# Kernel tuning notes

Measured on AMD Instinct MI355X. Metric: run time of the kernel, lower is better.

The kernel has to match this reference:

```python
import jax, jax.numpy as jnp
import numpy as np

B, S, U, H = 4, 2048, 1024, 16
DH = U // H  # head dim = 64
EPS = 1e-8


def setup_inputs() -> dict:
    key = jax.random.key(0)
    ks = jax.random.split(key, 7)
    scale = 1.0 / np.sqrt(U)
    return {
        "queries": jax.random.normal(ks[0], (B, S, U), jnp.float32),
        "keys": jax.random.normal(ks[1], (B, S, U), jnp.float32),
        "values": jax.random.normal(ks[2], (B, S, U), jnp.float32),
        "Wq": jax.random.normal(ks[3], (U, U), jnp.float32) * scale,
        "bq": jnp.zeros((U,), jnp.float32),
        "Wk": jax.random.normal(ks[4], (U, U), jnp.float32) * scale,
        "bk": jnp.zeros((U,), jnp.float32),
        "Wv": jax.random.normal(ks[5], (U, U), jnp.float32) * scale,
        "bv": jnp.zeros((U,), jnp.float32),
        "Wr": jax.random.normal(ks[6], (U, U), jnp.float32) * scale,
        "br": jnp.zeros((U,), jnp.float32),
        "gamma": jnp.ones((U,), jnp.float32),
        "beta": jnp.zeros((U,), jnp.float32),
    }


def reference(queries, keys, values, Wq, bq, Wk, bk, Wv, bv, Wr, br, gamma, beta):
    relu = jax.nn.relu
    Q = relu(queries @ Wq + bq)           # [B,S,U]
    K = relu(keys @ Wk + bk)
    V = relu(values @ Wv + bv)
    V_res = relu(values @ Wr + br)        # residual branch

    # split heads: tf.split(axis=2) + concat(axis=0) == per-head attention
    Qh = Q.reshape(B, S, H, DH)
    Kh = K.reshape(B, S, H, DH)
    Vh = V.reshape(B, S, H, DH)

    scores = jnp.einsum("bshd,bthd->bhst", Qh, Kh) / jnp.sqrt(jnp.float32(DH))
    w = jax.nn.softmax(scores, axis=-1)   # dropout keep_prob=1 -> identity
    out = jnp.einsum("bhst,bthd->bshd", w, Vh).reshape(B, S, U)

    out = relu(out + V_res)

    # manual LayerNorm (eps inside sqrt)
    mean = jnp.mean(out, axis=-1, keepdims=True)
    var = jnp.mean(jnp.square(out - mean), axis=-1, keepdims=True)
    normalized = (out - mean) / jnp.sqrt(var + EPS)
    return gamma * normalized + beta
```

## Files before the change

kernel.cpp:

```cpp
#include <hip/hip_runtime.h>

constexpr int B = 4, S = 2048, U = 1024, H = 16, DH = 64;
constexpr int MTOT = B * S;
constexpr int NT = S / 64;

using bf16   = __bf16;
using f32x4  = __attribute__((ext_vector_type(4))) float;
using f32x16 = __attribute__((ext_vector_type(16))) float;
using bf16x8 = __attribute__((ext_vector_type(8))) bf16;
using bf16x4 = __attribute__((ext_vector_type(4))) bf16;
using u32x4  = __attribute__((ext_vector_type(4))) unsigned int;

__device__ __forceinline__ void gload16(const bf16* g, bf16* l) {
  __builtin_amdgcn_global_load_lds(
      (const __attribute__((address_space(1))) unsigned int*)g,
      (__attribute__((address_space(3))) unsigned int*)l, 16, 0, 0);
}

__device__ __forceinline__ float fexp2(float x) {
#if __has_builtin(__builtin_amdgcn_exp2f)
  return __builtin_amdgcn_exp2f(x);
#else
  return __expf(x * 0.6931471805599453f);
#endif
}

__device__ __forceinline__ f32x16 mfma32(bf16x8 a, bf16x8 b, f32x16 c) {
  return __builtin_amdgcn_mfma_f32_32x32x16_bf16(a, b, c, 0, 0, 0);
}

__device__ __forceinline__ unsigned packbf(float a, float b) {
  union { bf16 h; unsigned short s; } ua, ub;
  ua.h = (bf16)a; ub.h = (bf16)b;
  return ((unsigned)ub.s << 16) | (unsigned)ua.s;
}

__device__ __forceinline__ size_t kpack_off(int M_, int col) {
  const int b = M_ >> 11, s = M_ & 2047;
  const int h = col >> 6, d = col & 63;
  const int bh = b * 16 + h;
  const int t = s >> 6, r64 = s & 63;
  const int tt = r64 >> 5, l31 = r64 & 31;
  const int ks = d >> 4, hi = (d >> 3) & 1, j = d & 7;
  const int ln = l31 + (hi << 5);
  return ((size_t)(bh * 32 + t) << 12) + (tt << 11) + (ks << 9) + (ln << 3) + j;
}

__device__ __forceinline__ size_t vpack_off(int M_, int col) {
  const int b = M_ >> 11, s = M_ & 2047;
  const int h = col >> 6, d = col & 63;
  const int bh = b * 16 + h;
  const int j = s & 7, hi = (s >> 3) & 1, ks = (s >> 4) & 3, t = s >> 6;
  const int dt = d >> 5, l31 = d & 31;
  const int ln = l31 + (hi << 5);
  return ((size_t)(bh * 32 + t) << 12) + (dt << 11) + (ks << 9) + (ln << 3) + j;
}

__global__ __launch_bounds__(256) void prep_kernel(
    const float* __restrict__ xq, const float* __restrict__ xk, const float* __restrict__ xv,
    bf16* __restrict__ oq, bf16* __restrict__ ok, bf16* __restrict__ ov,
    const float* __restrict__ w0, const float* __restrict__ w1,
    const float* __restrict__ w2, const float* __restrict__ w3,
    bf16* __restrict__ t0, bf16* __restrict__ t1,
    bf16* __restrict__ t2, bf16* __restrict__ t3) {
  __shared__ float tile[32][33];
  const int bid = blockIdx.x;
  const int t = threadIdx.x;
  if (bid < 12288) {
    const int z = bid >> 12, idx = bid & 4095;
    const float* x = z == 0 ? xq : z == 1 ? xk : xv;
    bf16* o       = z == 0 ? oq : z == 1 ? ok : ov;
    const size_t i = ((size_t)idx * 256 + t) * 8;
    const float4 v0 = *reinterpret_cast<const float4*>(x + i);
    const float4 v1 = *reinterpret_cast<const float4*>(x + i + 4);
    bf16x8 r;
    r[0] = (bf16)v0.x; r[1] = (bf16)v0.y; r[2] = (bf16)v0.z; r[3] = (bf16)v0.w;
    r[4] = (bf16)v1.x; r[5] = (bf16)v1.y; r[6] = (bf16)v1.z; r[7] = (bf16)v1.w;
    *reinterpret_cast<bf16x8*>(o + i) = r;
  } else {
    const int wb = bid - 12288;
    const int z = wb >> 10, ti = wb & 1023;
    const float* W = z == 0 ? w0 : z == 1 ? w1 : z == 2 ? w2 : w3;
    bf16* Wt       = z == 0 ? t0 : z == 1 ? t1 : z == 2 ? t2 : t3;
    const int k0 = (ti & 31) * 32, n0 = (ti >> 5) * 32;
    const int tx = t & 31, ty = t >> 5;
    for (int i = ty; i < 32; i += 8) tile[i][tx] = W[(size_t)(k0 + i) * U + n0 + tx];
    __syncthreads();
    for (int i = ty; i < 32; i += 8) Wt[(size_t)(n0 + i) * U + k0 + tx] = (bf16)tile[tx][i];
  }
}

__global__ __launch_bounds__(512, 2) void gemm4_kernel(
    const bf16* __restrict__ Qc, const bf16* __restrict__ Kc, const bf16* __restrict__ Vc,
    const bf16* __restrict__ wqt, const bf16* __restrict__ wkt,
    const bf16* __restrict__ wvt, const bf16* __restrict__ wrt,
    const float* __restrict__ bq, const float* __restrict__ bk,
    const float* __restrict__ bv, const float* __restrict__ br,
    bf16* __restrict__ oq, bf16* __restrict__ okp,
    bf16* __restrict__ ovp, bf16* __restrict__ orr) {
  const int bid = blockIdx.x;
  const int wg = (bid & 7) * 64 + (bid >> 3);
  const int z = wg >> 7, rem = wg & 127;
  const int bm = (rem >> 2) * 256, bn = (rem & 3) * 256;

  const bf16* A     = z == 0 ? Qc : z == 1 ? Kc : Vc;
  const bf16* Wt    = z == 0 ? wqt : z == 1 ? wkt : z == 2 ? wvt : wrt;
  const float* bias = z == 0 ? bq : z == 1 ? bk : z == 2 ? bv : br;

  const int tid = threadIdx.x, lane = tid & 63, w = tid >> 6;
  const int wr = w >> 2, wcn = w & 3;
  const int lm = lane & 15, hi = lane >> 4;

  __shared__ __align__(16) bf16 smem[65536];

  f32x4 acc[8][4];
#pragma unroll
  for (int i = 0; i < 8; ++i)
#pragma unroll
    for (int j = 0; j < 4; ++j) acc[i][j] = f32x4{0.f, 0.f, 0.f, 0.f};

  const int srow = tid >> 3, sslot = tid & 7;
  const int scol = (sslot ^ (srow & 7)) * 8;
  const bf16* gA = A  + (size_t)(bm + srow) * U + scol;
  const bf16* gB = Wt + (size_t)(bn + srow) * U + scol;

  auto stageA = [&](int buf, int half, int k0) {
    bf16* l = smem + buf * 32768 + (half * 128 + srow) * 64 + sslot * 8;
    gload16(gA + (size_t)(half * 128) * U + k0, l);
    gload16(gA + (size_t)(half * 128 + 64) * U + k0, l + 64 * 64);
  };
  auto stageB = [&](int buf, int half, int k0) {
    bf16* l = smem + buf * 32768 + 16384 + (half * 128 + srow) * 64 + sslot * 8;
    gload16(gB + (size_t)(half * 128) * U + k0, l);
    gload16(gB + (size_t)(half * 128 + 64) * U + k0, l + 64 * 64);
  };

  auto loadA = [&](int buf, int mi, int ks) {
    const int row = wr * 128 + mi * 16 + lm;
    const int slot = (ks * 4 + hi) ^ (lm & 7);
    return *reinterpret_cast<const bf16x8*>(smem + buf * 32768 + row * 64 + slot * 8);
  };
  auto loadB = [&](int buf, int ni, int ks) {
    const int row = wcn * 64 + ni * 16 + lm;
    const int slot = (ks * 4 + hi) ^ (lm & 7);
    return *reinterpret_cast<const bf16x8*>(smem + buf * 32768 + 16384 + row * 64 + slot * 8);
  };

  stageA(0, 0, 0); stageA(0, 1, 0); stageB(0, 0, 0); stageB(0, 1, 0);
  asm volatile("s_waitcnt vmcnt(0)" ::: "memory");
  __builtin_amdgcn_s_barrier();
  __builtin_amdgcn_sched_barrier(0);

  for (int t = 0; t < 16; ++t) {
    const int buf = t & 1, nbf = buf ^ 1;
    const int k1 = (t + 1) * 64;
    const bool pre = (t + 1) < 16;

    bf16x8 bfr[4][2];

    if (pre) stageA(nbf, 0, k1);
#pragma unroll
    for (int ni = 0; ni < 4; ++ni) {
      bfr[ni][0] = loadB(buf, ni, 0);
      bfr[ni][1] = loadB(buf, ni, 1);
    }
    {
      bf16x8 a00 = loadA(buf, 0, 0), a01 = loadA(buf, 0, 1);
      bf16x8 a10 = loadA(buf, 1, 0), a11 = loadA(buf, 1, 1);
      __builtin_amdgcn_s_setprio(1);
#pragma unroll
      for (int ni = 0; ni < 4; ++ni) {
        acc[0][ni] = __builtin_amdgcn_mfma_f32_16x16x32_bf16(a00, bfr[ni][0], acc[0][ni], 0, 0, 0);
        acc[0][ni] = __builtin_amdgcn_mfma_f32_16x16x32_bf16(a01, bfr[ni][1], acc[0][ni], 0, 0, 0);
        acc[1][ni] = __builtin_amdgcn_mfma_f32_16x16x32_bf16(a10, bfr[ni][0], acc[1][ni], 0, 0, 0);
        acc[1][ni] = __builtin_amdgcn_mfma_f32_16x16x32_bf16(a11, bfr[ni][1], acc[1][ni], 0, 0, 0);
      }
      __builtin_amdgcn_s_setprio(0);
    }
    if (pre) stageA(nbf, 1, k1);
    {
      bf16x8 a00 = loadA(buf, 2, 0), a01 = loadA(buf, 2, 1);
      bf16x8 a10 = loadA(buf, 3, 0), a11 = loadA(buf, 3, 1);
      __builtin_amdgcn_s_setprio(1);
#pragma unroll
      for (int ni = 0; ni < 4; ++ni) {
        acc[2][ni] = __builtin_amdgcn_mfma_f32_16x16x32_bf16(a00, bfr[ni][0], acc[2][ni], 0, 0, 0);
        acc[2][ni] = __builtin_amdgcn_mfma_f32_16x16x32_bf16(a01, bfr[ni][1], acc[2][ni], 0, 0, 0);
        acc[3][ni] = __builtin_amdgcn_mfma_f32_16x16x32_bf16(a10, bfr[ni][0], acc[3][ni], 0, 0, 0);
        acc[3][ni] = __builtin_amdgcn_mfma_f32_16x16x32_bf16(a11, bfr[ni][1], acc[3][ni], 0, 0, 0);
      }
      __builtin_amdgcn_s_setprio(0);
    }
    if (pre) stageB(nbf, 0, k1);
    {
      bf16x8 a00 = loadA(buf, 4, 0), a01 = loadA(buf, 4, 1);
      bf16x8 a10 = loadA(buf, 5, 0), a11 = loadA(buf, 5, 1);
      __builtin_amdgcn_s_setprio(1);
#pragma unroll
      for (int ni = 0; ni < 4; ++ni) {
        acc[4][ni] = __builtin_amdgcn_mfma_f32_16x16x32_bf16(a00, bfr[ni][0], acc[4][ni], 0, 0, 0);
        acc[4][ni] = __builtin_amdgcn_mfma_f32_16x16x32_bf16(a01, bfr[ni][1], acc[4][ni], 0, 0, 0);
        acc[5][ni] = __builtin_amdgcn_mfma_f32_16x16x32_bf16(a10, bfr[ni][0], acc[5][ni], 0, 0, 0);
        acc[5][ni] = __builtin_amdgcn_mfma_f32_16x16x32_bf16(a11, bfr[ni][1], acc[5][ni], 0, 0, 0);
      }
      __builtin_amdgcn_s_setprio(0);
    }
    if (pre) stageB(nbf, 1, k1);
    {
      bf16x8 a00 = loadA(buf, 6, 0), a01 = loadA(buf, 6, 1);
      bf16x8 a10 = loadA(buf, 7, 0), a11 = loadA(buf, 7, 1);
      __builtin_amdgcn_s_setprio(1);
#pragma unroll
      for (int ni = 0; ni < 4; ++ni) {
        acc[6][ni] = __builtin_amdgcn_mfma_f32_16x16x32_bf16(a00, bfr[ni][0], acc[6][ni], 0, 0, 0);
        acc[6][ni] = __builtin_amdgcn_mfma_f32_16x16x32_bf16(a01, bfr[ni][1], acc[6][ni], 0, 0, 0);
        acc[7][ni] = __builtin_amdgcn_mfma_f32_16x16x32_bf16(a10, bfr[ni][0], acc[7][ni], 0, 0, 0);
        acc[7][ni] = __builtin_amdgcn_mfma_f32_16x16x32_bf16(a11, bfr[ni][1], acc[7][ni], 0, 0, 0);
      }
      __builtin_amdgcn_s_setprio(0);
    }

    if (pre) {
      asm volatile("s_waitcnt vmcnt(0)" ::: "memory");
      __builtin_amdgcn_s_barrier();
      __builtin_amdgcn_sched_barrier(0);
    }
  }

  const int mb = bm + wr * 128 + hi * 4;
  const int nb = bn + wcn * 64 + lm;
  if (z == 1) {
#pragma unroll
    for (int ni = 0; ni < 4; ++ni) {
      const float bv_ = bias[nb + ni * 16];
#pragma unroll
      for (int mi = 0; mi < 8; ++mi)
#pragma unroll
        for (int r = 0; r < 4; ++r) {
          const float vv = fmaxf(acc[mi][ni][r] + bv_, 0.f);
          okp[kpack_off(mb + mi * 16 + r, nb + ni * 16)] = (bf16)vv;
        }
    }
  } else if (z == 2) {
#pragma unroll
    for (int ni = 0; ni < 4; ++ni) {
      const float bv_ = bias[nb + ni * 16];
#pragma unroll
      for (int mi = 0; mi < 8; ++mi)
#pragma unroll
        for (int r = 0; r < 4; ++r) {
          const float vv = fmaxf(acc[mi][ni][r] + bv_, 0.f);
          ovp[vpack_off(mb + mi * 16 + r, nb + ni * 16)] = (bf16)vv;
        }
    }
  } else {
    bf16* out = z == 0 ? oq : orr;
#pragma unroll
    for (int ni = 0; ni < 4; ++ni) {
      const float bv_ = bias[nb + ni * 16];
#pragma unroll
      for (int mi = 0; mi < 8; ++mi)
#pragma unroll
        for (int r = 0; r < 4; ++r) {
          const float vv = fmaxf(acc[mi][ni][r] + bv_, 0.f);
          out[(size_t)(mb + mi * 16 + r) * U + nb + ni * 16] = (bf16)vv;
        }
    }
  }
}

__global__ __launch_bounds__(256, 2) void attn_kernel(
    const bf16* __restrict__ Q, const bf16* __restrict__ Kp,
    const bf16* __restrict__ Vp, bf16* __restrict__ att) {
  const int bid = blockIdx.x;
  const int swz = (bid & 7) * 128 + (bid >> 3);
  const int bh = swz >> 4, qx = swz & 15;
  const int b = bh >> 4, h = bh & 15;
  const int tid = threadIdx.x;
  const int w = tid >> 6, lane = tid & 63;
  const int l31 = lane & 31, hi8 = lane >> 5;
  const int q0 = qx * 128 + w * 32;

  __shared__ __align__(16) bf16 kv[2][8192];

  const float qscale = 0.18033688011111606f;

  const bf16* qbase = Q + ((size_t)b * S + q0 + l31) * U + h * DH + hi8 * 8;
  bf16x8 qf[4];
#pragma unroll
  for (int ks = 0; ks < 4; ++ks) {
    bf16x8 v = *reinterpret_cast<const bf16x8*>(qbase + ks * 16);
#pragma unroll
    for (int j = 0; j < 8; ++j) v[j] = (bf16)((float)v[j] * qscale);
    qf[ks] = v;
  }

  bf16x8 onesf;
#pragma unroll
  for (int j = 0; j < 8; ++j) onesf[j] = (bf16)1.f;

  f32x16 o0 = (f32x16)0.f, o1 = (f32x16)0.f, osum = (f32x16)0.f;

  const bf16* kpb = Kp + (size_t)bh * 32 * 4096;
  const bf16* vpb = Vp + (size_t)bh * 32 * 4096;

  auto stagekv = [&](int buf, int t) {
    const size_t toff = (size_t)t * 4096;
    gload16(kpb + toff + tid * 8,        &kv[buf][tid * 8]);
    gload16(kpb + toff + 2048 + tid * 8, &kv[buf][2048 + tid * 8]);
    gload16(vpb + toff + tid * 8,        &kv[buf][4096 + tid * 8]);
    gload16(vpb + toff + 2048 + tid * 8, &kv[buf][6144 + tid * 8]);
  };

  stagekv(0, 0);
  asm volatile("s_waitcnt vmcnt(0)" ::: "memory");
  __builtin_amdgcn_s_barrier();
  __builtin_amdgcn_sched_barrier(0);

  for (int t = 0; t < NT; ++t) {
    const int cur = t & 1;
    if (t + 1 < NT) stagekv(cur ^ 1, t + 1);

    bf16x8 kf[2][4];
#pragma unroll
    for (int tt = 0; tt < 2; ++tt)
#pragma unroll
      for (int ks = 0; ks < 4; ++ks)
        kf[tt][ks] = *reinterpret_cast<const bf16x8*>(&kv[cur][(tt * 4 + ks) * 512 + lane * 8]);

    f32x16 s0 = (f32x16)0.f, s1 = (f32x16)0.f;
    __builtin_amdgcn_s_setprio(1);
#pragma unroll
    for (int ks = 0; ks < 4; ++ks) {
      s0 = mfma32(kf[0][ks], qf[ks], s0);
      s1 = mfma32(kf[1][ks], qf[ks], s1);
    }
    __builtin_amdgcn_s_setprio(0);

    bf16x8 vf[2][4];
#pragma unroll
    for (int dt = 0; dt < 2; ++dt)
#pragma unroll
      for (int ks = 0; ks < 4; ++ks)
        vf[dt][ks] = *reinterpret_cast<const bf16x8*>(&kv[cur][4096 + (dt * 4 + ks) * 512 + lane * 8]);

    unsigned wpk[16];
#pragma unroll
    for (int i = 0; i < 8; ++i) {
      wpk[i]     = packbf(fexp2(s0[2 * i]), fexp2(s0[2 * i + 1]));
      wpk[8 + i] = packbf(fexp2(s1[2 * i]), fexp2(s1[2 * i + 1]));
    }

    u32x4 fw[4];
#pragma unroll
    for (int fi = 0; fi < 4; ++fi) {
      unsigned a0 = wpk[fi * 4 + 0], b0 = wpk[fi * 4 + 2];
      unsigned a1 = wpk[fi * 4 + 1], b1 = wpk[fi * 4 + 3];
      asm("v_permlane32_swap_b32 %0, %1" : "+v"(a0), "+v"(b0));
      asm("v_permlane32_swap_b32 %0, %1" : "+v"(a1), "+v"(b1));
      fw[fi] = u32x4{a0, a1, b0, b1};
    }

    __builtin_amdgcn_s_setprio(1);
#pragma unroll
    for (int ks = 0; ks < 4; ++ks) {
      const bf16x8 pf = __builtin_bit_cast(bf16x8, fw[ks]);
      o0   = mfma32(pf, vf[0][ks], o0);
      o1   = mfma32(pf, vf[1][ks], o1);
      osum = mfma32(pf, onesf, osum);
    }
    __builtin_amdgcn_s_setprio(0);

    if (t + 1 < NT) {
      asm volatile("s_waitcnt vmcnt(0)" ::: "memory");
      __builtin_amdgcn_s_barrier();
      __builtin_amdgcn_sched_barrier(0);
    }
  }

  bf16* obase = att + ((size_t)b * S + q0) * U + h * DH + l31;
#pragma unroll
  for (int r = 0; r < 16; ++r) {
    const int row = (r & 3) + 8 * (r >> 2) + 4 * hi8;
    const float lr = 1.f / osum[r];
    obase[(size_t)row * U]      = (bf16)(o0[r] * lr);
    obase[(size_t)row * U + 32] = (bf16)(o1[r] * lr);
  }
}

__global__ __launch_bounds__(256) void ln_kernel(
    const bf16* __restrict__ att, const bf16* __restrict__ vres,
    const float* __restrict__ gamma, const float* __restrict__ beta,
    float* __restrict__ out) {
  const int w = threadIdx.x >> 6, lane = threadIdx.x & 63;
  const int row = blockIdx.x * 4 + w;
  const int c0 = lane * 16;
  const bf16* ar = att  + (size_t)row * U + c0;
  const bf16* vr = vres + (size_t)row * U + c0;

  const bf16x8 a0 = *reinterpret_cast<const bf16x8*>(ar);
  const bf16x8 a1 = *reinterpret_cast<const bf16x8*>(ar + 8);
  const bf16x8 v0 = *reinterpret_cast<const bf16x8*>(vr);
  const bf16x8 v1 = *reinterpret_cast<const bf16x8*>(vr + 8);

  float x[16];
  float sum = 0.f, sq = 0.f;
#pragma unroll
  for (int i = 0; i < 8; ++i) {
    x[i]     = fmaxf((float)a0[i] + (float)v0[i], 0.f);
    x[8 + i] = fmaxf((float)a1[i] + (float)v1[i], 0.f);
  }
#pragma unroll
  for (int i = 0; i < 16; ++i) { sum += x[i]; sq += x[i] * x[i]; }
#pragma unroll
  for (int mm = 1; mm < 64; mm <<= 1) {
    sum += __shfl_xor(sum, mm);
    sq  += __shfl_xor(sq, mm);
  }
  const float mean = sum * (1.f / U);
  float var = sq * (1.f / U) - mean * mean;
  var = fmaxf(var, 0.f);
  const float inv = rsqrtf(var + 1e-8f);

  float* orow = out + (size_t)row * U + c0;
#pragma unroll
  for (int j = 0; j < 4; ++j) {
    const float4 g = *reinterpret_cast<const float4*>(gamma + c0 + j * 4);
    const float4 bt = *reinterpret_cast<const float4*>(beta + c0 + j * 4);
    float4 o;
    o.x = g.x * ((x[j * 4 + 0] - mean) * inv) + bt.x;
    o.y = g.y * ((x[j * 4 + 1] - mean) * inv) + bt.y;
    o.z = g.z * ((x[j * 4 + 2] - mean) * inv) + bt.z;
    o.w = g.w * ((x[j * 4 + 3] - mean) * inv) + bt.w;
    *reinterpret_cast<float4*>(orow + j * 4) = o;
  }
}

extern "C" void kernel_launch(void* const* d_in, const int* in_sizes, int n_in,
                              void* d_out, int out_size, void* d_ws, size_t ws_size,
                              hipStream_t stream) {
  const float* queries = (const float*)d_in[0];
  const float* keys    = (const float*)d_in[1];
  const float* values  = (const float*)d_in[2];
  const float* Wq = (const float*)d_in[3];
  const float* bq = (const float*)d_in[4];
  const float* Wk = (const float*)d_in[5];
  const float* bk = (const float*)d_in[6];
  const float* Wv = (const float*)d_in[7];
  const float* bv = (const float*)d_in[8];
  const float* Wr = (const float*)d_in[9];
  const float* br = (const float*)d_in[10];
  const float* gamma = (const float*)d_in[11];
  const float* beta  = (const float*)d_in[12];
  float* out = (float*)d_out;

  char* ws = (char*)d_ws;
  const size_t MB = 1024 * 1024;
  bf16* wqt  = (bf16*)(ws + 0 * MB);
  bf16* wkt  = (bf16*)(ws + 2 * MB);
  bf16* wvt  = (bf16*)(ws + 4 * MB);
  bf16* wrt  = (bf16*)(ws + 6 * MB);
  bf16* Qcvt = (bf16*)(ws + 8 * MB);
  bf16* Kcvt = (bf16*)(ws + 24 * MB);
  bf16* Vcvt = (bf16*)(ws + 40 * MB);
  bf16* Qb   = (bf16*)(ws + 56 * MB);
  bf16* Kp   = (bf16*)(ws + 72 * MB);
  bf16* Vp   = (bf16*)(ws + 88 * MB);
  bf16* attb = Qcvt;
  bf16* Rb   = Kcvt;

  prep_kernel<<<dim3(16384), 256, 0, stream>>>(
      queries, keys, values, Qcvt, Kcvt, Vcvt,
      Wq, Wk, Wv, Wr, wqt, wkt, wvt, wrt);
  gemm4_kernel<<<dim3(512), 512, 0, stream>>>(
      Qcvt, Kcvt, Vcvt, wqt, wkt, wvt, wrt, bq, bk, bv, br, Qb, Kp, Vp, Rb);
  attn_kernel<<<dim3(1024), 256, 0, stream>>>(Qb, Kp, Vp, attb);
  ln_kernel<<<dim3(MTOT / 4), 256, 0, stream>>>(attb, Rb, gamma, beta, out);
}
```

Before: 201.5 us.

## Process two query groups per warp in attention and front-load GEMM staging

Each attention warp now handles 64 query rows as two 32-row groups that share the K and V fragments loaded from LDS. This halves the grid and halves K/V global traffic and LDS reads per query. Separately, the GEMM main loop issues all next-tile A and B global-to-LDS loads earlier in the iteration instead of spreading them across the four compute phases. The cost is higher register pressure from doubled accumulators and query fragments, fewer blocks (512 on a large GPU), and possibly less overlap in the GEMM.

```diff
diff --git a/kernel.cpp b/kernel.cpp
--- a/kernel.cpp
+++ b/kernel.cpp
@@ -158,7 +158,7 @@
 
     bf16x8 bfr[4][2];
 
-    if (pre) stageA(nbf, 0, k1);
+    if (pre) { stageA(nbf, 0, k1); stageA(nbf, 1, k1); }
 #pragma unroll
     for (int ni = 0; ni < 4; ++ni) {
       bfr[ni][0] = loadB(buf, ni, 0);
@@ -177,7 +177,7 @@
       }
       __builtin_amdgcn_s_setprio(0);
     }
-    if (pre) stageA(nbf, 1, k1);
+    if (pre) { stageB(nbf, 0, k1); stageB(nbf, 1, k1); }
     {
       bf16x8 a00 = loadA(buf, 2, 0), a01 = loadA(buf, 2, 1);
       bf16x8 a10 = loadA(buf, 3, 0), a11 = loadA(buf, 3, 1);
@@ -191,7 +191,6 @@
       }
       __builtin_amdgcn_s_setprio(0);
     }
-    if (pre) stageB(nbf, 0, k1);
     {
       bf16x8 a00 = loadA(buf, 4, 0), a01 = loadA(buf, 4, 1);
       bf16x8 a10 = loadA(buf, 5, 0), a11 = loadA(buf, 5, 1);
@@ -205,7 +204,6 @@
       }
       __builtin_amdgcn_s_setprio(0);
     }
-    if (pre) stageB(nbf, 1, k1);
     {
       bf16x8 a00 = loadA(buf, 6, 0), a01 = loadA(buf, 6, 1);
       bf16x8 a10 = loadA(buf, 7, 0), a11 = loadA(buf, 7, 1);
@@ -273,33 +271,40 @@
     const bf16* __restrict__ Q, const bf16* __restrict__ Kp,
     const bf16* __restrict__ Vp, bf16* __restrict__ att) {
   const int bid = blockIdx.x;
-  const int swz = (bid & 7) * 128 + (bid >> 3);
-  const int bh = swz >> 4, qx = swz & 15;
+  const int swz = (bid & 7) * 64 + (bid >> 3);
+  const int bh = swz >> 3, qx = swz & 7;
   const int b = bh >> 4, h = bh & 15;
   const int tid = threadIdx.x;
   const int w = tid >> 6, lane = tid & 63;
   const int l31 = lane & 31, hi8 = lane >> 5;
-  const int q0 = qx * 128 + w * 32;
+  const int q0 = qx * 256 + w * 64;
 
   __shared__ __align__(16) bf16 kv[2][8192];
 
   const float qscale = 0.18033688011111606f;
 
-  const bf16* qbase = Q + ((size_t)b * S + q0 + l31) * U + h * DH + hi8 * 8;
-  bf16x8 qf[4];
-#pragma unroll
-  for (int ks = 0; ks < 4; ++ks) {
-    bf16x8 v = *reinterpret_cast<const bf16x8*>(qbase + ks * 16);
-#pragma unroll
-    for (int j = 0; j < 8; ++j) v[j] = (bf16)((float)v[j] * qscale);
-    qf[ks] = v;
+  bf16x8 qf[2][4];
+#pragma unroll
+  for (int qg = 0; qg < 2; ++qg) {
+    const bf16* qbase = Q + ((size_t)b * S + q0 + qg * 32 + l31) * U + h * DH + hi8 * 8;
+#pragma unroll
+    for (int ks = 0; ks < 4; ++ks) {
+      bf16x8 v = *reinterpret_cast<const bf16x8*>(qbase + ks * 16);
+#pragma unroll
+      for (int j = 0; j < 8; ++j) v[j] = (bf16)((float)v[j] * qscale);
+      qf[qg][ks] = v;
+    }
   }
 
   bf16x8 onesf;
 #pragma unroll
   for (int j = 0; j < 8; ++j) onesf[j] = (bf16)1.f;
 
-  f32x16 o0 = (f32x16)0.f, o1 = (f32x16)0.f, osum = (f32x16)0.f;
+  f32x16 o[2][2], osum[2];
+#pragma unroll
+  for (int qg = 0; qg < 2; ++qg) {
+    o[qg][0] = (f32x16)0.f; o[qg][1] = (f32x16)0.f; osum[qg] = (f32x16)0.f;
+  }
 
   const bf16* kpb = Kp + (size_t)bh * 32 * 4096;
   const bf16* vpb = Vp + (size_t)bh * 32 * 4096;
@@ -321,53 +326,62 @@
     const int cur = t & 1;
     if (t + 1 < NT) stagekv(cur ^ 1, t + 1);
 
-    bf16x8 kf[2][4];
-#pragma unroll
-    for (int tt = 0; tt < 2; ++tt)
+    f32x16 s[2][2];
+    s[0][0] = (f32x16)0.f; s[0][1] = (f32x16)0.f;
+    s[1][0] = (f32x16)0.f; s[1][1] = (f32x16)0.f;
+#pragma unroll
+    for (int tt = 0; tt < 2; ++tt) {
+      bf16x8 kf4[4];
 #pragma unroll
       for (int ks = 0; ks < 4; ++ks)
-        kf[tt][ks] = *reinterpret_cast<const bf16x8*>(&kv[cur][(tt * 4 + ks) * 512 + lane * 8]);
-
-    f32x16 s0 = (f32x16)0.f, s1 = (f32x16)0.f;
+        kf4[ks] = *reinterpret_cast<const bf16x8*>(&kv[cur][(tt * 4 + ks) * 512 + lane * 8]);
+      __builtin_amdgcn_s_setprio(1);
+#pragma unroll
+      for (int ks = 0; ks < 4; ++ks) {
+        s[0][tt] = mfma32(kf4[ks], qf[0][ks], s[0][tt]);
+        s[1][tt] = mfma32(kf4[ks], qf[1][ks], s[1][tt]);
+      }
+      __builtin_amdgcn_s_setprio(0);
+    }
+
+    u32x4 fw[2][4];
+#pragma unroll
+    for (int qg = 0; qg < 2; ++qg) {
+      unsigned wpk[16];
+#pragma unroll
+      for (int i = 0; i < 8; ++i) {
+        wpk[i]     = packbf(fexp2(s[qg][0][2 * i]), fexp2(s[qg][0][2 * i + 1]));
+        wpk[8 + i] = packbf(fexp2(s[qg][1][2 * i]), fexp2(s[qg][1][2 * i + 1]));
+      }
+#pragma unroll
+      for (int fi = 0; fi < 4; ++fi) {
+        unsigned a0 = wpk[fi * 4 + 0], b0 = wpk[fi * 4 + 2];
+        unsigned a1 = wpk[fi * 4 + 1], b1 = wpk[fi * 4 + 3];
+        asm("v_permlane32_swap_b32 %0, %1" : "+v"(a0), "+v"(b0));
+        asm("v_permlane32_swap_b32 %0, %1" : "+v"(a1), "+v"(b1));
+        fw[qg][fi] = u32x4{a0, a1, b0, b1};
+      }
+    }
+
+#pragma unroll
+    for (int dt = 0; dt < 2; ++dt) {
+      bf16x8 vf4[4];
+#pragma unroll
+      for (int ks = 0; ks < 4; ++ks)
+        vf4[ks] = *reinterpret_cast<const bf16x8*>(&kv[cur][4096 + (dt * 4 + ks) * 512 + lane * 8]);
+      __builtin_amdgcn_s_setprio(1);
+#pragma unroll
+      for (int ks = 0; ks < 4; ++ks) {
+        o[0][dt] = mfma32(__builtin_bit_cast(bf16x8, fw[0][ks]), vf4[ks], o[0][dt]);
+        o[1][dt] = mfma32(__builtin_bit_cast(bf16x8, fw[1][ks]), vf4[ks], o[1][dt]);
+      }
+      __builtin_amdgcn_s_setprio(0);
+    }
     __builtin_amdgcn_s_setprio(1);
 #pragma unroll
     for (int ks = 0; ks < 4; ++ks) {
-      s0 = mfma32(kf[0][ks], qf[ks], s0);
-      s1 = mfma32(kf[1][ks], qf[ks], s1);
-    }
-    __builtin_amdgcn_s_setprio(0);
-
-    bf16x8 vf[2][4];
-#pragma unroll
-    for (int dt = 0; dt < 2; ++dt)
-#pragma unroll
-      for (int ks = 0; ks < 4; ++ks)
-        vf[dt][ks] = *reinterpret_cast<const bf16x8*>(&kv[cur][4096 + (dt * 4 + ks) * 512 + lane * 8]);
-
-    unsigned wpk[16];
-#pragma unroll
-    for (int i = 0; i < 8; ++i) {
-      wpk[i]     = packbf(fexp2(s0[2 * i]), fexp2(s0[2 * i + 1]));
-      wpk[8 + i] = packbf(fexp2(s1[2 * i]), fexp2(s1[2 * i + 1]));
-    }
-
-    u32x4 fw[4];
-#pragma unroll
-    for (int fi = 0; fi < 4; ++fi) {
-      unsigned a0 = wpk[fi * 4 + 0], b0 = wpk[fi * 4 + 2];
-      unsigned a1 = wpk[fi * 4 + 1], b1 = wpk[fi * 4 + 3];
-      asm("v_permlane32_swap_b32 %0, %1" : "+v"(a0), "+v"(b0));
-      asm("v_permlane32_swap_b32 %0, %1" : "+v"(a1), "+v"(b1));
-      fw[fi] = u32x4{a0, a1, b0, b1};
-    }
-
-    __builtin_amdgcn_s_setprio(1);
-#pragma unroll
-    for (int ks = 0; ks < 4; ++ks) {
-      const bf16x8 pf = __builtin_bit_cast(bf16x8, fw[ks]);
-      o0   = mfma32(pf, vf[0][ks], o0);
-      o1   = mfma32(pf, vf[1][ks], o1);
-      osum = mfma32(pf, onesf, osum);
+      osum[0] = mfma32(__builtin_bit_cast(bf16x8, fw[0][ks]), onesf, osum[0]);
+      osum[1] = mfma32(__builtin_bit_cast(bf16x8, fw[1][ks]), onesf, osum[1]);
     }
     __builtin_amdgcn_s_setprio(0);
 
@@ -378,13 +392,16 @@
     }
   }
 
-  bf16* obase = att + ((size_t)b * S + q0) * U + h * DH + l31;
-#pragma unroll
-  for (int r = 0; r < 16; ++r) {
-    const int row = (r & 3) + 8 * (r >> 2) + 4 * hi8;
-    const float lr = 1.f / osum[r];
-    obase[(size_t)row * U]      = (bf16)(o0[r] * lr);
-    obase[(size_t)row * U + 32] = (bf16)(o1[r] * lr);
+#pragma unroll
+  for (int qg = 0; qg < 2; ++qg) {
+    bf16* obase = att + ((size_t)b * S + q0 + qg * 32) * U + h * DH + l31;
+#pragma unroll
+    for (int r = 0; r < 16; ++r) {
+      const int row = (r & 3) + 8 * (r >> 2) + 4 * hi8;
+      const float lr = 1.f / osum[qg][r];
+      obase[(size_t)row * U]      = (bf16)(o[qg][0][r] * lr);
+      obase[(size_t)row * U + 32] = (bf16)(o[qg][1][r] * lr);
+    }
   }
 }
 
@@ -474,6 +491,6 @@
       Wq, Wk, Wv, Wr, wqt, wkt, wvt, wrt);
   gemm4_kernel<<<dim3(512), 512, 0, stream>>>(
       Qcvt, Kcvt, Vcvt, wqt, wkt, wvt, wrt, bq, bk, bv, br, Qb, Kp, Vp, Rb);
-  attn_kernel<<<dim3(1024), 256, 0, stream>>>(Qb, Kp, Vp, attb);
+  attn_kernel<<<dim3(512), 256, 0, stream>>>(Qb, Kp, Vp, attb);
   ln_kernel<<<dim3(MTOT / 4), 256, 0, stream>>>(attb, Rb, gamma, beta, out);
 }
```

Result: no change. 199.3 us (-1.1%).
